# Performance work log

Hardware: AMD Instinct MI355X
Metric: run time of the kernel (lower is better)

## Reference

```python
import jax, jax.numpy as jnp
import numpy as np

B, C_IN, IMG, P = 64, 3, 224, 16
GRID = IMG // P              # 14
N_PATCH = GRID * GRID        # 196
S = N_PATCH + 1              # 197 tokens incl CLS
D, H, HD = 768, 12, 64
DFF = 3072
L, PRUNE_AFTER = 12, 4
RATIO, EPS = 0.5, 1e-6
NEG = -1e30                  # additive mask value (softmax weight -> exactly 0 in fp32)
N_CLASSES = 1000
N_KEEP = max(1, int(S * (1.0 - RATIO)))  # 98, matches torch topk count


def _ln(x, g, b):
    m = x.mean(-1, keepdims=True)
    v = ((x - m) ** 2).mean(-1, keepdims=True)
    return (x - m) * jax.lax.rsqrt(v + EPS) * g + b


def _attn(x, qkv_w, qkv_b, proj_w, proj_b, amask):
    Bx, N, C = x.shape
    qkv = (x @ qkv_w.T + qkv_b).reshape(Bx, N, 3, H, HD).transpose(2, 0, 3, 1, 4)
    q, k, v = qkv[0], qkv[1], qkv[2]            # [B,H,N,HD]
    s = jnp.einsum('bhqd,bhkd->bhqk', q, k) * (HD ** -0.5)
    if amask is not None:
        s = s + amask                            # [B,1,1,N] broadcast
    a = jax.nn.softmax(s, axis=-1)
    o = jnp.einsum('bhqk,bhkd->bhqd', a, v).transpose(0, 2, 1, 3).reshape(Bx, N, C)
    return o @ proj_w.T + proj_b


def _block(x, i, p, amask=None):
    h = _ln(x, p['ln1_g'][i], p['ln1_b'][i])
    x = x + _attn(h, p['qkv_w'][i], p['qkv_b'][i], p['proj_w'][i], p['proj_b'][i], amask)
    h = _ln(x, p['ln2_g'][i], p['ln2_b'][i])
    h = jax.nn.gelu(h @ p['fc1_w'][i].T + p['fc1_b'][i], approximate=False)
    x = x + (h @ p['fc2_w'][i].T + p['fc2_b'][i])
    return x


def _forward(images, patch_w, patch_b, cls_token, pos_embed,
             ln1_g, ln1_b, qkv_w, qkv_b, proj_w, proj_b,
             ln2_g, ln2_b, fc1_w, fc1_b, fc2_w, fc2_b,
             norm_g, norm_b, head_w, head_b):
    p = dict(ln1_g=ln1_g, ln1_b=ln1_b, qkv_w=qkv_w, qkv_b=qkv_b,
             proj_w=proj_w, proj_b=proj_b, ln2_g=ln2_g, ln2_b=ln2_b,
             fc1_w=fc1_w, fc1_b=fc1_b, fc2_w=fc2_w, fc2_b=fc2_b)
    Bx = images.shape[0]
    # patch embed: non-overlapping 16x16 conv == patch extract + matmul
    patches = images.reshape(Bx, C_IN, GRID, P, GRID, P).transpose(0, 2, 4, 1, 3, 5)
    patches = patches.reshape(Bx, N_PATCH, C_IN * P * P)
    x = patches @ patch_w.reshape(D, -1).T + patch_b          # [B,196,768]
    x = jnp.concatenate([jnp.broadcast_to(cls_token, (Bx, 1, D)), x], axis=1)
    x = x + pos_embed                                          # [B,197,768]
    # early dense blocks
    for i in range(PRUNE_AFTER):
        x = _block(x, i, p)
    # _threshold_prune: topk on token norms, CLS always kept
    scores = jnp.linalg.norm(x, axis=-1)                       # [B,S]
    _, idx = jax.lax.top_k(scores, N_KEEP)                     # [B,98]
    mask = jnp.zeros((Bx, S), bool).at[jnp.arange(Bx)[:, None], idx].set(True)
    mask = mask.at[:, 0].set(True)
    # _gather_pad: kept tokens compacted to front (original order), zeros after
    order = jnp.argsort(~mask, axis=1, stable=True)            # True positions first
    x_pad = jnp.take_along_axis(x, order[:, :, None], axis=1)
    attn_m = jnp.take_along_axis(mask, order, axis=1)          # [B,S] True-prefix
    x_pad = x_pad * attn_m[:, :, None]
    amask = jnp.where(attn_m, 0.0, NEG).astype(x.dtype)[:, None, None, :]  # [B,1,1,S]
    # late masked blocks
    for i in range(PRUNE_AFTER, L):
        x_pad = _block(x_pad, i, p, amask)
    cls = _ln(x_pad[:, 0], norm_g, norm_b)
    return cls @ head_w.T + head_b                             # [B,1000]


def setup_inputs():
    key = jax.random.key(0)
    ks = iter(jax.random.split(key, 32))
    r = lambda shape: jax.random.normal(next(ks), shape, jnp.float32) * 0.02
    return {
        'images': jax.random.normal(next(ks), (B, C_IN, IMG, IMG), jnp.float32),
        'patch_w': r((D, C_IN, P, P)),
        'patch_b': r((D,)),
        'cls_token': r((1, 1, D)),
        'pos_embed': r((1, S, D)),
        'ln1_g': jnp.ones((L, D), jnp.float32),
        'ln1_b': jnp.zeros((L, D), jnp.float32),
        'qkv_w': r((L, 3 * D, D)),
        'qkv_b': r((L, 3 * D)),
        'proj_w': r((L, D, D)),
        'proj_b': r((L, D)),
        'ln2_g': jnp.ones((L, D), jnp.float32),
        'ln2_b': jnp.zeros((L, D), jnp.float32),
        'fc1_w': r((L, DFF, D)),
        'fc1_b': r((L, DFF)),
        'fc2_w': r((L, D, DFF)),
        'fc2_b': r((L, D)),
        'norm_g': jnp.ones((D,), jnp.float32),
        'norm_b': jnp.zeros((D,), jnp.float32),
        'head_w': r((N_CLASSES, D)),
        'head_b': r((N_CLASSES,)),
    }


def reference(images, patch_w, patch_b, cls_token, pos_embed,
              ln1_g, ln1_b, qkv_w, qkv_b, proj_w, proj_b,
              ln2_g, ln2_b, fc1_w, fc1_b, fc2_w, fc2_b,
              norm_g, norm_b, head_w, head_b):
    return _forward(images, patch_w, patch_b, cls_token, pos_embed,
                    ln1_g, ln1_b, qkv_w, qkv_b, proj_w, proj_b,
                    ln2_g, ln2_b, fc1_w, fc1_b, fc2_w, fc2_b,
                    norm_g, norm_b, head_w, head_b)
```

## Files before the change

kernel.cpp:

```cpp
#include <hip/hip_runtime.h>
#include <cstdint>
#include <cstddef>


#define NTOK 197
#define NB 64
#define NHEAD 12
#define SL 99

typedef __attribute__((ext_vector_type(8))) _Float16 half8;
typedef __attribute__((ext_vector_type(4))) float f32x4;
typedef __attribute__((ext_vector_type(4))) unsigned short us4;

#define DEV static __device__ __forceinline__

DEV unsigned short f2h(float f) {
    union { _Float16 h; unsigned short u; } v;
    v.h = (_Float16)f;
    return v.u;
}
DEV float h2f(unsigned short u) {
    union { _Float16 h; unsigned short u; } v;
    v.u = u;
    return (float)v.h;
}

DEV void gload16(const void* g, void* l) {
    __builtin_amdgcn_global_load_lds((const __attribute__((address_space(1))) unsigned int*)g,
                                     (__attribute__((address_space(3))) unsigned int*)l, 16, 0, 0);
}

__global__ __launch_bounds__(256) void cvt_layer4_k(const float* __restrict__ qw,
                                                    const float* __restrict__ pw,
                                                    const float* __restrict__ f1,
                                                    const float* __restrict__ f2,
                                                    int i0,
                                                    unsigned short* __restrict__ dst)
{
    int l = blockIdx.x / 6912;
    int b2 = blockIdx.x % 6912;
    int li = i0 + l;
    size_t t = (size_t)b2 * 256 + threadIdx.x;
    size_t e = t * 4;
    const float* src; size_t loc;
    if (e < 1769472)      { src = qw + (size_t)li * 1769472; loc = e; }
    else if (e < 2359296) { src = pw + (size_t)li * 589824;  loc = e - 1769472; }
    else if (e < 4718592) { src = f1 + (size_t)li * 2359296; loc = e - 2359296; }
    else                  { src = f2 + (size_t)li * 2359296; loc = e - 4718592; }
    float4 v = *(const float4*)(src + loc);
    us4 hi; hi.x = f2h(v.x); hi.y = f2h(v.y); hi.z = f2h(v.z); hi.w = f2h(v.w);
    *(us4*)(dst + (size_t)l * 7077888 + e) = hi;
}

__global__ __launch_bounds__(256) void cvt_simple_k(const float* __restrict__ src,
                                                    unsigned short* __restrict__ dh, int n4)
{
    int t = blockIdx.x * 256 + threadIdx.x;
    if (t >= n4) return;
    size_t e = (size_t)t * 4;
    float4 v = *(const float4*)(src + e);
    us4 hi; hi.x = f2h(v.x); hi.y = f2h(v.y); hi.z = f2h(v.z); hi.w = f2h(v.w);
    *(us4*)(dh + e) = hi;
}

__global__ __launch_bounds__(256) void patch_extract2_k(const float* __restrict__ img,
                                                        unsigned short* __restrict__ ph)
{
    int pi = blockIdx.x, b = blockIdx.y;
    int gy = pi / 14, gx = pi % 14;
    size_t obase = ((size_t)b * 196 + pi) * 768;
    for (int f = threadIdx.x; f < 768; f += 256) {
        int c = f >> 8, py = (f >> 4) & 15, px = f & 15;
        float v = img[(((size_t)b * 3 + c) * 224 + gy * 16 + py) * 224 + gx * 16 + px];
        ph[obase + f] = f2h(v);
    }
}

__global__ __launch_bounds__(256) void assemble_k(const unsigned short* __restrict__ emb,
                                                  const float* __restrict__ cls,
                                                  const float* __restrict__ pos,
                                                  unsigned short* __restrict__ x)
{
    int s = blockIdx.x, b = blockIdx.y;
    size_t xo = ((size_t)b * NTOK + s) * 768;
    for (int d = threadIdx.x; d < 768; d += 256) {
        float v = (s == 0) ? cls[d] : h2f(emb[((size_t)b * 196 + (s - 1)) * 768 + d]);
        x[xo + d] = f2h(v + pos[(size_t)s * 768 + d]);
    }
}

__global__ __launch_bounds__(256) void ln2_k(const unsigned short* __restrict__ in,
                                             unsigned short* __restrict__ outh,
                                             const float* __restrict__ g,
                                             const float* __restrict__ bt, size_t ldin)
{
    const unsigned short* xr = in + (size_t)blockIdx.x * ldin;
    size_t ob = (size_t)blockIdx.x * 768;
    int t = threadIdx.x;
    float v0 = h2f(xr[t]), v1 = h2f(xr[t + 256]), v2 = h2f(xr[t + 512]);
    float s = v0 + v1 + v2;
#pragma unroll
    for (int o = 32; o; o >>= 1) s += __shfl_xor(s, o);
    __shared__ float r1[4], r2[4];
    int wv = t >> 6, ln = t & 63;
    if (ln == 0) r1[wv] = s;
    __syncthreads();
    float mean = (r1[0] + r1[1] + r1[2] + r1[3]) * (1.f / 768.f);
    float d0 = v0 - mean, d1 = v1 - mean, d2 = v2 - mean;
    float ss = d0 * d0 + d1 * d1 + d2 * d2;
#pragma unroll
    for (int o = 32; o; o >>= 1) ss += __shfl_xor(ss, o);
    if (ln == 0) r2[wv] = ss;
    __syncthreads();
    float inv = rsqrtf((r2[0] + r2[1] + r2[2] + r2[3]) * (1.f / 768.f) + 1e-6f);
    outh[ob + t]       = f2h(d0 * inv * g[t]       + bt[t]);
    outh[ob + t + 256] = f2h(d1 * inv * g[t + 256] + bt[t + 256]);
    outh[ob + t + 512] = f2h(d2 * inv * g[t + 512] + bt[t + 512]);
}

template<int EPI, int OS, int MAP>
__global__ __launch_bounds__(256) void mgemm_k(const unsigned short* __restrict__ Ah,
                                               const unsigned short* __restrict__ Wh,
                                               const float* __restrict__ bias,
                                               const unsigned short* __restrict__ res,
                                               unsigned short* __restrict__ Chi,
                                               float* __restrict__ Cf,
                                               int M, int N, int K, int nR, int nC, int nRloc)
{
    __shared__ unsigned short lds[3 * 8192];

    int rt, ct;
    {
        int bid = blockIdx.x;
        if (MAP == 0) { rt = bid % nR; ct = bid / nR; }
        else {
            int xcd = bid & 7, u = bid >> 3, rl, c;
            if (MAP == 3) { rl = u % nRloc; c = u / nRloc; }
            else          { c = u % nC;     rl = u / nC;   }
            rt = xcd * nRloc + rl; ct = c;
            if (rt >= nR) return;
        }
    }
    const int row0 = rt << 7, col0 = ct << 7;
    const int tid = threadIdx.x;
    const int w = tid >> 6, lane = tid & 63;
    const int wr = w >> 1, wc = w & 1;
    const int srow = lane >> 2;
    const int schunk = ((lane & 3) ^ ((srow >> 1) & 3)) << 3;
    const int fr = lane & 15, fq = lane >> 4;
    const int rchunk = (fq ^ ((fr >> 1) & 3)) << 3;

    f32x4 acc[4][4];
#pragma unroll
    for (int m = 0; m < 4; m++)
#pragma unroll
        for (int n = 0; n < 4; n++) acc[m][n] = (f32x4)0.f;

    const int nk = K >> 5;

    auto stage = [&](int t, int slot) {
        const int k0 = t << 5;
        unsigned short* Ad = lds + slot * 8192;
        unsigned short* Bd = Ad + 4096;
#pragma unroll
        for (int i = 0; i < 2; i++) {
            int r = i * 64 + w * 16 + srow;
            int ga = row0 + r; if (ga > M - 1) ga = M - 1;
            int gb = col0 + r; if (gb > N - 1) gb = N - 1;
            gload16(Ah + (size_t)ga * K + k0 + schunk, Ad + i * 2048 + w * 512);
            gload16(Wh + (size_t)gb * K + k0 + schunk, Bd + i * 2048 + w * 512);
        }
    };

    stage(0, 0);
    stage(1, 1);
    int slot = 0, slot2 = 2;
    for (int t = 0; t < nk; ++t) {
        if (t + 1 < nk) asm volatile("s_waitcnt vmcnt(4)" ::: "memory");
        else            asm volatile("s_waitcnt vmcnt(0)" ::: "memory");
        __builtin_amdgcn_s_barrier();
        if (t + 2 < nk) stage(t + 2, slot2);
        const unsigned short* Ab = lds + slot * 8192;
        const unsigned short* Bb = Ab + 4096;
        half8 a[4], bb[4];
#pragma unroll
        for (int m = 0; m < 4; m++)
            a[m] = *(const half8*)(Ab + (wr * 64 + m * 16 + fr) * 32 + rchunk);
#pragma unroll
        for (int n = 0; n < 4; n++)
            bb[n] = *(const half8*)(Bb + (wc * 64 + n * 16 + fr) * 32 + rchunk);
#pragma unroll
        for (int m = 0; m < 4; m++)
#pragma unroll
            for (int n = 0; n < 4; n++)
                acc[m][n] = __builtin_amdgcn_mfma_f32_16x16x32_f16(a[m], bb[n], acc[m][n], 0, 0, 0);
        slot = (slot == 2) ? 0 : slot + 1;
        slot2 = (slot2 == 2) ? 0 : slot2 + 1;
    }

#pragma unroll
    for (int m = 0; m < 4; m++) {
#pragma unroll
        for (int n = 0; n < 4; n++) {
            int col = col0 + wc * 64 + n * 16 + fr;
#pragma unroll
            for (int r = 0; r < 4; r++) {
                int row = row0 + wr * 64 + m * 16 + fq * 4 + r;
                if (row < M && col < N) {
                    float v = acc[m][n][r] + bias[col];
                    size_t o = (size_t)row * N + col;
                    if (EPI == 2) v += h2f(res[o]);
                    if (EPI == 1) v = 0.5f * v * (1.f + erff(v * 0.70710678118654752f));
                    if (OS == 0) Cf[o] = v;
                    else Chi[o] = f2h(v);
                }
            }
        }
    }
}

template<int S, int KT, int PVKT, int PSTR>
__global__ __launch_bounds__(256) void attn2_k(const unsigned short* __restrict__ qh,
                                               unsigned short* __restrict__ oh,
                                               const int* __restrict__ cntp)
{
    constexpr int PVK = PVKT * 32;
    constexpr int QT = (S + 15) / 16;
    extern __shared__ unsigned short sh[];
    unsigned short* VT = sh;
    unsigned short* PL = sh + 64 * PSTR;

    const int h = blockIdx.x, b = blockIdx.y;
    const int tid = threadIdx.x, w = tid >> 6, lane = tid & 63;
    const int nk = cntp ? cntp[b] : S;
    const size_t qbase = (size_t)b * S * 2304 + (size_t)h * 64;
    const int fr = lane & 15, fq = lane >> 4;

    for (int j0 = 0; j0 < S; j0 += 32) {
        int j = j0 + (tid >> 3);
        int d8 = (tid & 7) * 8;
        if (j < S) {
            size_t src = qbase + (size_t)j * 2304 + 1536 + d8;
            us4 v0 = *(const us4*)(qh + src);
            us4 v1 = *(const us4*)(qh + src + 4);
            VT[(d8 + 0) * PSTR + j] = v0.x; VT[(d8 + 1) * PSTR + j] = v0.y;
            VT[(d8 + 2) * PSTR + j] = v0.z; VT[(d8 + 3) * PSTR + j] = v0.w;
            VT[(d8 + 4) * PSTR + j] = v1.x; VT[(d8 + 5) * PSTR + j] = v1.y;
            VT[(d8 + 6) * PSTR + j] = v1.z; VT[(d8 + 7) * PSTR + j] = v1.w;
        }
    }
    for (int idx = tid; idx < 64 * (PVK - S); idx += 256) {
        int d = idx / (PVK - S), j = S + idx % (PVK - S);
        VT[d * PSTR + j] = 0;
    }
    {
        unsigned short* Pw = PL + w * 16 * PSTR;
        for (int idx = lane; idx < 16 * (PVK - 16 * KT); idx += 64) {
            int rr = idx / (PVK - 16 * KT), cc = 16 * KT + idx % (PVK - 16 * KT);
            Pw[rr * PSTR + cc] = 0;
        }
    }
    __syncthreads();

    for (int qt = w; qt < QT; qt += 4) {
        int qr = qt * 16 + fr; int qrc = qr < S ? qr : S - 1;
        const size_t qrow = qbase + (size_t)qrc * 2304;
        half8 qf0[2];
#pragma unroll
        for (int ks = 0; ks < 2; ks++)
            qf0[ks] = *(const half8*)(qh + qrow + ks * 32 + fq * 8);
        f32x4 sc[KT];
#pragma unroll
        for (int kt = 0; kt < KT; kt++) {
            int ky = kt * 16 + fr; int kyc = ky < S ? ky : S - 1;
            const size_t krow = qbase + (size_t)kyc * 2304 + 768;
            f32x4 acc = (f32x4)0.f;
#pragma unroll
            for (int ks = 0; ks < 2; ks++) {
                half8 kh = *(const half8*)(qh + krow + ks * 32 + fq * 8);
                acc = __builtin_amdgcn_mfma_f32_16x16x32_f16(qf0[ks], kh, acc, 0, 0, 0);
            }
            sc[kt] = acc;
        }
        float mx[4] = {-3e38f, -3e38f, -3e38f, -3e38f};
#pragma unroll
        for (int kt = 0; kt < KT; kt++) {
            bool valid = (kt * 16 + fr) < nk;
#pragma unroll
            for (int r = 0; r < 4; r++) {
                float s = sc[kt][r] * 0.125f;
                sc[kt][r] = s;
                if (valid) mx[r] = fmaxf(mx[r], s);
            }
        }
#pragma unroll
        for (int off = 1; off < 16; off <<= 1)
#pragma unroll
            for (int r = 0; r < 4; r++) mx[r] = fmaxf(mx[r], __shfl_xor(mx[r], off));
        float sum[4] = {0.f, 0.f, 0.f, 0.f};
#pragma unroll
        for (int kt = 0; kt < KT; kt++) {
            bool valid = (kt * 16 + fr) < nk;
#pragma unroll
            for (int r = 0; r < 4; r++) {
                float p = valid ? __expf(sc[kt][r] - mx[r]) : 0.f;
                sc[kt][r] = p;
                sum[r] += p;
            }
        }
#pragma unroll
        for (int off = 1; off < 16; off <<= 1)
#pragma unroll
            for (int r = 0; r < 4; r++) sum[r] += __shfl_xor(sum[r], off);
        float inv[4];
#pragma unroll
        for (int r = 0; r < 4; r++) inv[r] = 1.f / sum[r];
        unsigned short* Pw = PL + w * 16 * PSTR;
#pragma unroll
        for (int kt = 0; kt < KT; kt++) {
#pragma unroll
            for (int r = 0; r < 4; r++)
                Pw[(fq * 4 + r) * PSTR + kt * 16 + fr] = f2h(sc[kt][r] * inv[r]);
        }
        f32x4 o[4];
#pragma unroll
        for (int n = 0; n < 4; n++) o[n] = (f32x4)0.f;
#pragma unroll
        for (int ks = 0; ks < PVKT; ks++) {
            half8 pa = *(const half8*)(Pw + fr * PSTR + ks * 32 + fq * 8);
#pragma unroll
            for (int n = 0; n < 4; n++) {
                half8 vb = *(const half8*)(VT + (n * 16 + fr) * PSTR + ks * 32 + fq * 8);
                o[n] = __builtin_amdgcn_mfma_f32_16x16x32_f16(pa, vb, o[n], 0, 0, 0);
            }
        }
#pragma unroll
        for (int n = 0; n < 4; n++) {
#pragma unroll
            for (int r = 0; r < 4; r++) {
                int row = qt * 16 + fq * 4 + r;
                if (row < S) {
                    size_t oidx = ((size_t)b * S + row) * 768 + (size_t)h * 64 + n * 16 + fr;
                    oh[oidx] = f2h(o[n][r]);
                }
            }
        }
    }
}

__global__ __launch_bounds__(256) void normsq_k(const unsigned short* __restrict__ x,
                                                float* __restrict__ norms)
{
    const unsigned short* xr = x + (size_t)blockIdx.x * 768;
    int t = threadIdx.x;
    float v0 = h2f(xr[t]), v1 = h2f(xr[t + 256]), v2 = h2f(xr[t + 512]);
    float ss = v0 * v0 + v1 * v1 + v2 * v2;
#pragma unroll
    for (int o = 32; o; o >>= 1) ss += __shfl_xor(ss, o);
    __shared__ float r1[4];
    if ((t & 63) == 0) r1[t >> 6] = ss;
    __syncthreads();
    if (t == 0) norms[blockIdx.x] = r1[0] + r1[1] + r1[2] + r1[3];
}

__global__ __launch_bounds__(256) void topk_k(const float* __restrict__ norms,
                                              int* __restrict__ idxmap, int* __restrict__ cnt)
{
    int b = blockIdx.x, t = threadIdx.x;
    __shared__ float n[NTOK];
    __shared__ unsigned char kp[NTOK];
    if (t < NTOK) n[t] = norms[b * NTOK + t];
    __syncthreads();
    if (t < NTOK) {
        float me = n[t];
        int rank = 0;
        for (int j = 0; j < NTOK; j++) rank += (n[j] > me) || (n[j] == me && j < t);
        kp[t] = (rank < 98) || (t == 0);
    }
    __syncthreads();
    if (t == 0) {
        int c = 0;
        for (int s = 0; s < NTOK; s++) if (kp[s]) idxmap[b * SL + c++] = s;
        cnt[b] = c;
        for (int j = c; j < SL; j++) idxmap[b * SL + j] = 0;
    }
}

__global__ __launch_bounds__(256) void gather_k(const unsigned short* __restrict__ x,
                                                const int* __restrict__ idxmap,
                                                const int* __restrict__ cnt,
                                                unsigned short* __restrict__ xl)
{
    int j = blockIdx.x, b = blockIdx.y;
    size_t dst = ((size_t)b * SL + j) * 768;
    if (j < cnt[b]) {
        int s = idxmap[b * SL + j];
        size_t src = ((size_t)b * NTOK + s) * 768;
        for (int d = threadIdx.x; d < 768; d += 256) xl[dst + d] = x[src + d];
    } else {
        for (int d = threadIdx.x; d < 768; d += 256) xl[dst + d] = 0;
    }
}

extern "C" void kernel_launch(void* const* d_in, const int* in_sizes, int n_in,
                              void* d_out, int out_size, void* d_ws, size_t ws_size,
                              hipStream_t stream)
{
    const float* images  = (const float*)d_in[0];
    const float* patch_w = (const float*)d_in[1];
    const float* patch_b = (const float*)d_in[2];
    const float* cls_tok = (const float*)d_in[3];
    const float* pos_emb = (const float*)d_in[4];
    const float* ln1_g   = (const float*)d_in[5];
    const float* ln1_b   = (const float*)d_in[6];
    const float* qkv_w   = (const float*)d_in[7];
    const float* qkv_b   = (const float*)d_in[8];
    const float* proj_w  = (const float*)d_in[9];
    const float* proj_b  = (const float*)d_in[10];
    const float* ln2_g   = (const float*)d_in[11];
    const float* ln2_b   = (const float*)d_in[12];
    const float* fc1_w   = (const float*)d_in[13];
    const float* fc1_b   = (const float*)d_in[14];
    const float* fc2_w   = (const float*)d_in[15];
    const float* fc2_b   = (const float*)d_in[16];
    const float* norm_g  = (const float*)d_in[17];
    const float* norm_b  = (const float*)d_in[18];
    const float* head_w  = (const float*)d_in[19];
    const float* head_b  = (const float*)d_in[20];
    float* outp = (float*)d_out;

    char* W = (char*)d_ws;
    unsigned short* x16  = (unsigned short*)W;
    unsigned short* hbh  = (unsigned short*)(W + 19365888);
    char* R = W + 38731776;
    unsigned short* ph   = (unsigned short*)R;
    unsigned short* emb  = (unsigned short*)(R + 19365888);
    unsigned short* qkh  = (unsigned short*)R;
    unsigned short* ffh  = (unsigned short*)R;
    unsigned short* xl16 = (unsigned short*)(W + 116195328);
    unsigned short* wb4  = (unsigned short*)(W + 125927424);
    unsigned short* pwh  = (unsigned short*)(W + 182550528);
    unsigned short* hwb  = (unsigned short*)(W + 183730176);
    float* norms         = (float*)(W + 185303040);
    unsigned short* clsb = (unsigned short*)(W + 185353472);
    int* idxmap          = (int*)(W + 185451776);
    int* cnt             = (int*)(W + 185477120);

    const int LDS_EARLY = (64 * 232 + 4 * 16 * 232) * 2;
    const int LDS_LATE  = (64 * 136 + 4 * 16 * 136) * 2;
    (void)hipFuncSetAttribute(reinterpret_cast<const void*>(&attn2_k<197, 13, 7, 232>),
                              hipFuncAttributeMaxDynamicSharedMemorySize, LDS_EARLY);
    (void)hipFuncSetAttribute(reinterpret_cast<const void*>(&attn2_k<99, 7, 4, 136>),
                              hipFuncAttributeMaxDynamicSharedMemorySize, LDS_LATE);

    const int nR1 = 99, nRl1 = 13;
    const int nRp = 98, nRlp = 13;
    const int nR2 = 50, nRl2 = 7;

    cvt_simple_k<<<576, 256, 0, stream>>>(patch_w, pwh, 147456);
    patch_extract2_k<<<dim3(196, NB), 256, 0, stream>>>(images, ph);
    mgemm_k<0, 1, 3><<<8 * nRlp * 6, 256, 0, stream>>>(ph, pwh, patch_b, nullptr,
        emb, nullptr, 12544, 768, 768, nRp, 6, nRlp);
    assemble_k<<<dim3(NTOK, NB), 256, 0, stream>>>(emb, cls_tok, pos_emb, x16);

    const int M1 = NB * NTOK;
    for (int i = 0; i < 4; i++) {
        if (i == 0)
            cvt_layer4_k<<<4 * 6912, 256, 0, stream>>>(qkv_w, proj_w, fc1_w, fc2_w, 0, wb4);
        unsigned short* wbh = wb4 + (size_t)(i & 3) * 7077888;
        ln2_k<<<M1, 256, 0, stream>>>(x16, hbh, ln1_g + (size_t)i * 768, ln1_b + (size_t)i * 768, 768);
        mgemm_k<0, 1, 3><<<8 * nRl1 * 18, 256, 0, stream>>>(hbh, wbh,
            qkv_b + (size_t)i * 2304, nullptr, qkh, nullptr, M1, 2304, 768, nR1, 18, nRl1);
        attn2_k<197, 13, 7, 232><<<dim3(NHEAD, NB), 256, LDS_EARLY, stream>>>(qkh, hbh, nullptr);
        mgemm_k<2, 1, 3><<<8 * nRl1 * 6, 256, 0, stream>>>(hbh, wbh + 1769472,
            proj_b + (size_t)i * 768, x16, x16, nullptr, M1, 768, 768, nR1, 6, nRl1);
        ln2_k<<<M1, 256, 0, stream>>>(x16, hbh, ln2_g + (size_t)i * 768, ln2_b + (size_t)i * 768, 768);
        mgemm_k<1, 1, 3><<<8 * nRl1 * 24, 256, 0, stream>>>(hbh, wbh + 2359296,
            fc1_b + (size_t)i * 3072, nullptr, ffh, nullptr, M1, 3072, 768, nR1, 24, nRl1);
        mgemm_k<2, 1, 4><<<8 * nRl1 * 6, 256, 0, stream>>>(ffh, wbh + 4718592,
            fc2_b + (size_t)i * 768, x16, x16, nullptr, M1, 768, 3072, nR1, 6, nRl1);
    }

    normsq_k<<<M1, 256, 0, stream>>>(x16, norms);
    topk_k<<<NB, 256, 0, stream>>>(norms, idxmap, cnt);
    gather_k<<<dim3(SL, NB), 256, 0, stream>>>(x16, idxmap, cnt, xl16);

    const int M2 = NB * SL;
    for (int i = 4; i < 12; i++) {
        if (i == 4)
            cvt_layer4_k<<<4 * 6912, 256, 0, stream>>>(qkv_w, proj_w, fc1_w, fc2_w, 4, wb4);
        if (i == 8)
            cvt_layer4_k<<<4 * 6912, 256, 0, stream>>>(qkv_w, proj_w, fc1_w, fc2_w, 8, wb4);
        unsigned short* wbh = wb4 + (size_t)(i & 3) * 7077888;
        ln2_k<<<M2, 256, 0, stream>>>(xl16, hbh, ln1_g + (size_t)i * 768, ln1_b + (size_t)i * 768, 768);
        mgemm_k<0, 1, 3><<<8 * nRl2 * 18, 256, 0, stream>>>(hbh, wbh,
            qkv_b + (size_t)i * 2304, nullptr, qkh, nullptr, M2, 2304, 768, nR2, 18, nRl2);
        attn2_k<99, 7, 4, 136><<<dim3(NHEAD, NB), 256, LDS_LATE, stream>>>(qkh, hbh, cnt);
        mgemm_k<2, 1, 3><<<8 * nRl2 * 6, 256, 0, stream>>>(hbh, wbh + 1769472,
            proj_b + (size_t)i * 768, xl16, xl16, nullptr, M2, 768, 768, nR2, 6, nRl2);
        ln2_k<<<M2, 256, 0, stream>>>(xl16, hbh, ln2_g + (size_t)i * 768, ln2_b + (size_t)i * 768, 768);
        mgemm_k<1, 1, 3><<<8 * nRl2 * 24, 256, 0, stream>>>(hbh, wbh + 2359296,
            fc1_b + (size_t)i * 3072, nullptr, ffh, nullptr, M2, 3072, 768, nR2, 24, nRl2);
        mgemm_k<2, 1, 4><<<8 * nRl2 * 6, 256, 0, stream>>>(ffh, wbh + 4718592,
            fc2_b + (size_t)i * 768, xl16, xl16, nullptr, M2, 768, 3072, nR2, 6, nRl2);
    }

    ln2_k<<<NB, 256, 0, stream>>>(xl16, clsb, norm_g, norm_b, (size_t)SL * 768);
    cvt_simple_k<<<750, 256, 0, stream>>>(head_w, hwb, 192000);
    mgemm_k<0, 0, 0><<<8, 256, 0, stream>>>(clsb, hwb,
        head_b, nullptr, nullptr, outp, 64, 1000, 768, 1, 8, 1);
}
```

Baseline: 3.846 ms.

## Use single-wave vectorized LayerNorm/norm/gather, fast GELU approximation, and MFMA setprio

LayerNorm, the token-norm kernel and gather now use one 64-thread wave per row with 12-element vector loads and stores, so the shared-memory cross-wave reductions and their barriers go away. The exact erff in the fc1 GELU epilogue is replaced by the Abramowitz-Stegun polynomial erf approximation, which uses a hardware reciprocal and exp and introduces small numerical error. The attention kernel raises wave priority around its MFMA loops with s_setprio to favour matrix work. These changes target overhead in memory-bound elementwise kernels and the GEMM epilogue.

```diff
diff --git a/kernel.cpp b/kernel.cpp
--- a/kernel.cpp
+++ b/kernel.cpp
@@ -28,6 +28,17 @@
 DEV void gload16(const void* g, void* l) {
     __builtin_amdgcn_global_load_lds((const __attribute__((address_space(1))) unsigned int*)g,
                                      (__attribute__((address_space(3))) unsigned int*)l, 16, 0, 0);
+}
+
+DEV float gelu_f(float v) {
+    float x = v * 0.70710678118654752f;
+    float ax = fabsf(x);
+    float t = __builtin_amdgcn_rcpf(fmaf(0.3275911f, ax, 1.0f));
+    float poly = fmaf(fmaf(fmaf(fmaf(1.061405429f, t, -1.453152027f), t,
+                               1.421413741f), t, -0.284496736f), t, 0.254829592f) * t;
+    float erf_ax = 1.0f - poly * __expf(-x * x);
+    float er = (x < 0.f) ? -erf_ax : erf_ax;
+    return 0.5f * v * (1.0f + er);
 }
 
 __global__ __launch_bounds__(256) void cvt_layer4_k(const float* __restrict__ qw,
@@ -89,33 +100,50 @@
     }
 }
 
-__global__ __launch_bounds__(256) void ln2_k(const unsigned short* __restrict__ in,
-                                             unsigned short* __restrict__ outh,
-                                             const float* __restrict__ g,
-                                             const float* __restrict__ bt, size_t ldin)
+__global__ __launch_bounds__(64) void lnw_k(const unsigned short* __restrict__ in,
+                                            unsigned short* __restrict__ outh,
+                                            const float* __restrict__ g,
+                                            const float* __restrict__ bt, size_t ldin)
 {
     const unsigned short* xr = in + (size_t)blockIdx.x * ldin;
     size_t ob = (size_t)blockIdx.x * 768;
-    int t = threadIdx.x;
-    float v0 = h2f(xr[t]), v1 = h2f(xr[t + 256]), v2 = h2f(xr[t + 512]);
-    float s = v0 + v1 + v2;
+    const int t = threadIdx.x;
+    const int e0 = t * 12;
+
+    us4 a = *(const us4*)(xr + e0);
+    us4 b = *(const us4*)(xr + e0 + 4);
+    us4 c = *(const us4*)(xr + e0 + 8);
+    float v[12];
+    v[0] = h2f(a.x); v[1] = h2f(a.y); v[2]  = h2f(a.z); v[3]  = h2f(a.w);
+    v[4] = h2f(b.x); v[5] = h2f(b.y); v[6]  = h2f(b.z); v[7]  = h2f(b.w);
+    v[8] = h2f(c.x); v[9] = h2f(c.y); v[10] = h2f(c.z); v[11] = h2f(c.w);
+
+    float s = 0.f;
+#pragma unroll
+    for (int e = 0; e < 12; e++) s += v[e];
 #pragma unroll
     for (int o = 32; o; o >>= 1) s += __shfl_xor(s, o);
-    __shared__ float r1[4], r2[4];
-    int wv = t >> 6, ln = t & 63;
-    if (ln == 0) r1[wv] = s;
-    __syncthreads();
-    float mean = (r1[0] + r1[1] + r1[2] + r1[3]) * (1.f / 768.f);
-    float d0 = v0 - mean, d1 = v1 - mean, d2 = v2 - mean;
-    float ss = d0 * d0 + d1 * d1 + d2 * d2;
+    float mean = s * (1.f / 768.f);
+    float ss = 0.f;
+#pragma unroll
+    for (int e = 0; e < 12; e++) { float d = v[e] - mean; ss += d * d; }
 #pragma unroll
     for (int o = 32; o; o >>= 1) ss += __shfl_xor(ss, o);
-    if (ln == 0) r2[wv] = ss;
-    __syncthreads();
-    float inv = rsqrtf((r2[0] + r2[1] + r2[2] + r2[3]) * (1.f / 768.f) + 1e-6f);
-    outh[ob + t]       = f2h(d0 * inv * g[t]       + bt[t]);
-    outh[ob + t + 256] = f2h(d1 * inv * g[t + 256] + bt[t + 256]);
-    outh[ob + t + 512] = f2h(d2 * inv * g[t + 512] + bt[t + 512]);
+    float inv = rsqrtf(ss * (1.f / 768.f) + 1e-6f);
+
+    float4 g0 = *(const float4*)(g + e0),  g1 = *(const float4*)(g + e0 + 4),  g2 = *(const float4*)(g + e0 + 8);
+    float4 b0 = *(const float4*)(bt + e0), b1 = *(const float4*)(bt + e0 + 4), b2 = *(const float4*)(bt + e0 + 8);
+    float gg[12] = {g0.x,g0.y,g0.z,g0.w, g1.x,g1.y,g1.z,g1.w, g2.x,g2.y,g2.z,g2.w};
+    float bb[12] = {b0.x,b0.y,b0.z,b0.w, b1.x,b1.y,b1.z,b1.w, b2.x,b2.y,b2.z,b2.w};
+    unsigned short o16[12];
+#pragma unroll
+    for (int e = 0; e < 12; e++) o16[e] = f2h((v[e] - mean) * inv * gg[e] + bb[e]);
+    us4 oa = {o16[0], o16[1], o16[2],  o16[3]};
+    us4 obv = {o16[4], o16[5], o16[6],  o16[7]};
+    us4 oc = {o16[8], o16[9], o16[10], o16[11]};
+    *(us4*)(outh + ob + e0)     = oa;
+    *(us4*)(outh + ob + e0 + 4) = obv;
+    *(us4*)(outh + ob + e0 + 8) = oc;
 }
 
 template<int EPI, int OS, int MAP>
@@ -210,7 +238,7 @@
                     float v = acc[m][n][r] + bias[col];
                     size_t o = (size_t)row * N + col;
                     if (EPI == 2) v += h2f(res[o]);
-                    if (EPI == 1) v = 0.5f * v * (1.f + erff(v * 0.70710678118654752f));
+                    if (EPI == 1) v = gelu_f(v);
                     if (OS == 0) Cf[o] = v;
                     else Chi[o] = f2h(v);
                 }
@@ -270,6 +298,7 @@
         for (int ks = 0; ks < 2; ks++)
             qf0[ks] = *(const half8*)(qh + qrow + ks * 32 + fq * 8);
         f32x4 sc[KT];
+        __builtin_amdgcn_s_setprio(1);
 #pragma unroll
         for (int kt = 0; kt < KT; kt++) {
             int ky = kt * 16 + fr; int kyc = ky < S ? ky : S - 1;
@@ -282,6 +311,7 @@
             }
             sc[kt] = acc;
         }
+        __builtin_amdgcn_s_setprio(0);
         float mx[4] = {-3e38f, -3e38f, -3e38f, -3e38f};
 #pragma unroll
         for (int kt = 0; kt < KT; kt++) {
@@ -325,6 +355,7 @@
         f32x4 o[4];
 #pragma unroll
         for (int n = 0; n < 4; n++) o[n] = (f32x4)0.f;
+        __builtin_amdgcn_s_setprio(1);
 #pragma unroll
         for (int ks = 0; ks < PVKT; ks++) {
             half8 pa = *(const half8*)(Pw + fr * PSTR + ks * 32 + fq * 8);
@@ -334,6 +365,7 @@
                 o[n] = __builtin_amdgcn_mfma_f32_16x16x32_f16(pa, vb, o[n], 0, 0, 0);
             }
         }
+        __builtin_amdgcn_s_setprio(0);
 #pragma unroll
         for (int n = 0; n < 4; n++) {
 #pragma unroll
@@ -348,19 +380,26 @@
     }
 }
 
-__global__ __launch_bounds__(256) void normsq_k(const unsigned short* __restrict__ x,
-                                                float* __restrict__ norms)
+__global__ __launch_bounds__(64) void normsq_k(const unsigned short* __restrict__ x,
+                                               float* __restrict__ norms)
 {
     const unsigned short* xr = x + (size_t)blockIdx.x * 768;
-    int t = threadIdx.x;
-    float v0 = h2f(xr[t]), v1 = h2f(xr[t + 256]), v2 = h2f(xr[t + 512]);
-    float ss = v0 * v0 + v1 * v1 + v2 * v2;
+    const int t = threadIdx.x;
+    const int e0 = t * 12;
+    us4 a = *(const us4*)(xr + e0);
+    us4 b = *(const us4*)(xr + e0 + 4);
+    us4 c = *(const us4*)(xr + e0 + 8);
+    float ss = 0.f;
+    float v;
+    v = h2f(a.x); ss += v * v; v = h2f(a.y); ss += v * v;
+    v = h2f(a.z); ss += v * v; v = h2f(a.w); ss += v * v;
+    v = h2f(b.x); ss += v * v; v = h2f(b.y); ss += v * v;
+    v = h2f(b.z); ss += v * v; v = h2f(b.w); ss += v * v;
+    v = h2f(c.x); ss += v * v; v = h2f(c.y); ss += v * v;
+    v = h2f(c.z); ss += v * v; v = h2f(c.w); ss += v * v;
 #pragma unroll
     for (int o = 32; o; o >>= 1) ss += __shfl_xor(ss, o);
-    __shared__ float r1[4];
-    if ((t & 63) == 0) r1[t >> 6] = ss;
-    __syncthreads();
-    if (t == 0) norms[blockIdx.x] = r1[0] + r1[1] + r1[2] + r1[3];
+    if (t == 0) norms[blockIdx.x] = ss;
 }
 
 __global__ __launch_bounds__(256) void topk_k(const float* __restrict__ norms,
@@ -386,19 +425,26 @@
     }
 }
 
-__global__ __launch_bounds__(256) void gather_k(const unsigned short* __restrict__ x,
-                                                const int* __restrict__ idxmap,
-                                                const int* __restrict__ cnt,
-                                                unsigned short* __restrict__ xl)
+__global__ __launch_bounds__(64) void gather_k(const unsigned short* __restrict__ x,
+                                               const int* __restrict__ idxmap,
+                                               const int* __restrict__ cnt,
+                                               unsigned short* __restrict__ xl)
 {
     int j = blockIdx.x, b = blockIdx.y;
     size_t dst = ((size_t)b * SL + j) * 768;
+    const int t = threadIdx.x;
+    const int e0 = t * 12;
     if (j < cnt[b]) {
         int s = idxmap[b * SL + j];
         size_t src = ((size_t)b * NTOK + s) * 768;
-        for (int d = threadIdx.x; d < 768; d += 256) xl[dst + d] = x[src + d];
+        *(us4*)(xl + dst + e0)     = *(const us4*)(x + src + e0);
+        *(us4*)(xl + dst + e0 + 4) = *(const us4*)(x + src + e0 + 4);
+        *(us4*)(xl + dst + e0 + 8) = *(const us4*)(x + src + e0 + 8);
     } else {
-        for (int d = threadIdx.x; d < 768; d += 256) xl[dst + d] = 0;
+        us4 z = {0, 0, 0, 0};
+        *(us4*)(xl + dst + e0)     = z;
+        *(us4*)(xl + dst + e0 + 4) = z;
+        *(us4*)(xl + dst + e0 + 8) = z;
     }
 }
 
@@ -468,22 +514,22 @@
         if (i == 0)
             cvt_layer4_k<<<4 * 6912, 256, 0, stream>>>(qkv_w, proj_w, fc1_w, fc2_w, 0, wb4);
         unsigned short* wbh = wb4 + (size_t)(i & 3) * 7077888;
-        ln2_k<<<M1, 256, 0, stream>>>(x16, hbh, ln1_g + (size_t)i * 768, ln1_b + (size_t)i * 768, 768);
+        lnw_k<<<M1, 64, 0, stream>>>(x16, hbh, ln1_g + (size_t)i * 768, ln1_b + (size_t)i * 768, 768);
         mgemm_k<0, 1, 3><<<8 * nRl1 * 18, 256, 0, stream>>>(hbh, wbh,
             qkv_b + (size_t)i * 2304, nullptr, qkh, nullptr, M1, 2304, 768, nR1, 18, nRl1);
         attn2_k<197, 13, 7, 232><<<dim3(NHEAD, NB), 256, LDS_EARLY, stream>>>(qkh, hbh, nullptr);
         mgemm_k<2, 1, 3><<<8 * nRl1 * 6, 256, 0, stream>>>(hbh, wbh + 1769472,
             proj_b + (size_t)i * 768, x16, x16, nullptr, M1, 768, 768, nR1, 6, nRl1);
-        ln2_k<<<M1, 256, 0, stream>>>(x16, hbh, ln2_g + (size_t)i * 768, ln2_b + (size_t)i * 768, 768);
+        lnw_k<<<M1, 64, 0, stream>>>(x16, hbh, ln2_g + (size_t)i * 768, ln2_b + (size_t)i * 768, 768);
         mgemm_k<1, 1, 3><<<8 * nRl1 * 24, 256, 0, stream>>>(hbh, wbh + 2359296,
             fc1_b + (size_t)i * 3072, nullptr, ffh, nullptr, M1, 3072, 768, nR1, 24, nRl1);
         mgemm_k<2, 1, 4><<<8 * nRl1 * 6, 256, 0, stream>>>(ffh, wbh + 4718592,
             fc2_b + (size_t)i * 768, x16, x16, nullptr, M1, 768, 3072, nR1, 6, nRl1);
     }
 
-    normsq_k<<<M1, 256, 0, stream>>>(x16, norms);
+    normsq_k<<<M1, 64, 0, stream>>>(x16, norms);
     topk_k<<<NB, 256, 0, stream>>>(norms, idxmap, cnt);
-    gather_k<<<dim3(SL, NB), 256, 0, stream>>>(x16, idxmap, cnt, xl16);
+    gather_k<<<dim3(SL, NB), 64, 0, stream>>>(x16, idxmap, cnt, xl16);
 
     const int M2 = NB * SL;
     for (int i = 4; i < 12; i++) {
@@ -492,20 +538,20 @@
         if (i == 8)
             cvt_layer4_k<<<4 * 6912, 256, 0, stream>>>(qkv_w, proj_w, fc1_w, fc2_w, 8, wb4);
         unsigned short* wbh = wb4 + (size_t)(i & 3) * 7077888;
-        ln2_k<<<M2, 256, 0, stream>>>(xl16, hbh, ln1_g + (size_t)i * 768, ln1_b + (size_t)i * 768, 768);
+        lnw_k<<<M2, 64, 0, stream>>>(xl16, hbh, ln1_g + (size_t)i * 768, ln1_b + (size_t)i * 768, 768);
         mgemm_k<0, 1, 3><<<8 * nRl2 * 18, 256, 0, stream>>>(hbh, wbh,
             qkv_b + (size_t)i * 2304, nullptr, qkh, nullptr, M2, 2304, 768, nR2, 18, nRl2);
         attn2_k<99, 7, 4, 136><<<dim3(NHEAD, NB), 256, LDS_LATE, stream>>>(qkh, hbh, cnt);
         mgemm_k<2, 1, 3><<<8 * nRl2 * 6, 256, 0, stream>>>(hbh, wbh + 1769472,
             proj_b + (size_t)i * 768, xl16, xl16, nullptr, M2, 768, 768, nR2, 6, nRl2);
-        ln2_k<<<M2, 256, 0, stream>>>(xl16, hbh, ln2_g + (size_t)i * 768, ln2_b + (size_t)i * 768, 768);
+        lnw_k<<<M2, 64, 0, stream>>>(xl16, hbh, ln2_g + (size_t)i * 768, ln2_b + (size_t)i * 768, 768);
         mgemm_k<1, 1, 3><<<8 * nRl2 * 24, 256, 0, stream>>>(hbh, wbh + 2359296,
             fc1_b + (size_t)i * 3072, nullptr, ffh, nullptr, M2, 3072, 768, nR2, 24, nRl2);
         mgemm_k<2, 1, 4><<<8 * nRl2 * 6, 256, 0, stream>>>(ffh, wbh + 4718592,
             fc2_b + (size_t)i * 768, xl16, xl16, nullptr, M2, 768, 3072, nR2, 6, nRl2);
     }
 
-    ln2_k<<<NB, 256, 0, stream>>>(xl16, clsb, norm_g, norm_b, (size_t)SL * 768);
+    lnw_k<<<NB, 64, 0, stream>>>(xl16, clsb, norm_g, norm_b, (size_t)SL * 768);
     cvt_simple_k<<<750, 256, 0, stream>>>(head_w, hwb, 192000);
     mgemm_k<0, 0, 0><<<8, 256, 0, stream>>>(clsb, hwb,
         head_b, nullptr, nullptr, outp, 64, 1000, 768, 1, 8, 1);
```

Result: faster. 3.732 ms (median of 2 runs) (-3.0%).
